# Optimization experiments

Measured on AMD Instinct MI355X. Metric: run time of the kernel, lower is better.

The kernel has to match this reference:

```python
import jax, jax.numpy as jnp
import numpy as np

B, H, L, D = 4, 16, 2048, 64


def setup_inputs() -> dict:
    key = jax.random.key(0)
    k1, k2, k3 = jax.random.split(key, 3)
    return {
        "query": jax.random.normal(k1, (B, H, L, D), dtype=jnp.float32),
        "key": jax.random.normal(k2, (B, H, L, D), dtype=jnp.float32),
        "value": jax.random.normal(k3, (B, H, D, L), dtype=jnp.float32),
    }


def reference(query, key, value):
    # dot_product_score = Q @ K^T / sqrt(D)   -> [B,H,L,L]
    d = query.shape[-1]
    scores = jnp.einsum("bhqd,bhkd->bhqk", query, key) / jnp.sqrt(jnp.asarray(d, query.dtype))
    attn = jax.nn.softmax(scores, axis=-1)
    # NOTE: original module returns matmul(value, attention_score) = V @ A
    # (value contracted over its last dim L with attn's query dim L) -> [B,H,D,L]
    return jnp.matmul(value, attn)
```

## Files before the change

### kernel.cpp

```cpp
#include <hip/hip_runtime.h>
#include <hip/hip_bf16.h>

#define L_SEQ 2048
#define D_HEAD 64
#define NHEADS 64
#define QSCALE (0.125f * 1.44269504088896340736f)

typedef __attribute__((ext_vector_type(8))) __bf16 bf16x8;
typedef __attribute__((ext_vector_type(16))) float f32x16;

__device__ __forceinline__ int swz(int row, int col) {
    int off = (row << 7) | (col << 1);
    return off ^ ((row & 7) << 4);
}
__device__ __forceinline__ bf16x8 read_frag(const char* lds, int row, int col) {
    return *reinterpret_cast<const bf16x8*>(lds + swz(row, col));
}

template <int ROWS>
__device__ __forceinline__ void stage_load(float4* regs, const float* src,
                                           int srcStride, int t) {
    int r0 = t >> 4, c4 = (t & 15) << 2;
#pragma unroll
    for (int i = 0; i < ROWS / 16; ++i)
        regs[i] = *reinterpret_cast<const float4*>(src + (size_t)(r0 + i * 16) * srcStride + c4);
}
template <int ROWS>
__device__ __forceinline__ void stage_write(char* lds, const float4* regs, int t,
                                            float scale) {
    int r0 = t >> 4, c4 = (t & 15) << 2;
#pragma unroll
    for (int i = 0; i < ROWS / 16; ++i) {
        float4 v = regs[i];
        union { __bf16 h[4]; unsigned long long u; } pk;
        pk.h[0] = (__bf16)(v.x * scale);
        pk.h[1] = (__bf16)(v.y * scale);
        pk.h[2] = (__bf16)(v.z * scale);
        pk.h[3] = (__bf16)(v.w * scale);
        *reinterpret_cast<unsigned long long*>(lds + swz(r0 + i * 16, c4)) = pk.u;
    }
}

__device__ __forceinline__ void pack_write(char* lds, int row, int c4, float4 v,
                                           float4 sc) {
    union { __bf16 h[4]; unsigned long long u; } pk;
    pk.h[0] = (__bf16)(v.x * sc.x);
    pk.h[1] = (__bf16)(v.y * sc.y);
    pk.h[2] = (__bf16)(v.z * sc.z);
    pk.h[3] = (__bf16)(v.w * sc.w);
    *reinterpret_cast<unsigned long long*>(lds + swz(row, c4)) = pk.u;
}

__device__ __forceinline__ unsigned cvt_pk_bf16(float lo, float hi) {
    unsigned r;
    asm("v_cvt_pk_bf16_f32 %0, %1, %2" : "=v"(r) : "v"(lo), "v"(hi));
    return r;
}

__global__ __launch_bounds__(256, 3) void attn_pass1(const float* __restrict__ Q,
                                                     const float* __restrict__ K,
                                                     float* __restrict__ invl) {
    __shared__ __align__(16) char lds[2][128 * 128];
    __shared__ float red[4][64];

    int bid = blockIdx.x;
    int sb = (bid & 7) * 256 + (bid >> 3);
    int bh = sb >> 5;
    int q0 = (sb & 31) << 6;
    const float* Qh = Q + (size_t)bh * L_SEQ * D_HEAD + (size_t)q0 * D_HEAD;
    const float* Kh = K + (size_t)bh * L_SEQ * D_HEAD;

    int t = threadIdx.x, lane = t & 63, w = t >> 6;
    int hl = lane >> 5, l31 = lane & 31;

    {
        float4 qreg[4];
        stage_load<64>(qreg, Qh, D_HEAD, t);
        stage_write<64>(lds[0], qreg, t, QSCALE);
    }
    __syncthreads();
    bf16x8 qfrag[2][4];
#pragma unroll
    for (int qb = 0; qb < 2; ++qb)
#pragma unroll
        for (int m = 0; m < 4; ++m)
            qfrag[qb][m] = read_frag(lds[0], qb * 32 + l31, m * 16 + hl * 8);
    __syncthreads();
    {
        float4 kreg[8];
        stage_load<128>(kreg, Kh, D_HEAD, t);
        stage_write<128>(lds[0], kreg, t, 1.0f);
    }
    __syncthreads();

    float lsum[2][16];
#pragma unroll
    for (int qb = 0; qb < 2; ++qb)
#pragma unroll
        for (int r = 0; r < 16; ++r) lsum[qb][r] = 0.f;

    for (int k0 = 0; k0 < L_SEQ; k0 += 128) {
        int c = (k0 >> 7) & 1;
        const char* kcur = lds[c];
        char* knext = lds[c ^ 1];

        int nk0 = (k0 + 128) & (L_SEQ - 1);
        float4 kreg[8];
        stage_load<128>(kreg, Kh + (size_t)nk0 * D_HEAD, D_HEAD, t);

        bf16x8 kfr[4];
#pragma unroll
        for (int m = 0; m < 4; ++m)
            kfr[m] = read_frag(kcur, w * 32 + l31, m * 16 + hl * 8);

        f32x16 s[2];
#pragma unroll
        for (int qb = 0; qb < 2; ++qb)
#pragma unroll
            for (int r = 0; r < 16; ++r) s[qb][r] = 0.f;

        __builtin_amdgcn_s_setprio(1);
#pragma unroll
        for (int m = 0; m < 4; ++m) {
            s[0] = __builtin_amdgcn_mfma_f32_32x32x16_bf16(qfrag[0][m], kfr[m], s[0], 0, 0, 0);
            s[1] = __builtin_amdgcn_mfma_f32_32x32x16_bf16(qfrag[1][m], kfr[m], s[1], 0, 0, 0);
        }
        __builtin_amdgcn_s_setprio(0);

#pragma unroll
        for (int qb = 0; qb < 2; ++qb)
#pragma unroll
            for (int r = 0; r < 16; ++r)
                lsum[qb][r] += __builtin_amdgcn_exp2f(s[qb][r]);

        stage_write<128>(knext, kreg, t, 1.0f);
        __syncthreads();
    }

#pragma unroll
    for (int qb = 0; qb < 2; ++qb)
#pragma unroll
        for (int r = 0; r < 16; ++r) {
            float v = lsum[qb][r];
            v += __shfl_xor(v, 1);
            v += __shfl_xor(v, 2);
            v += __shfl_xor(v, 4);
            v += __shfl_xor(v, 8);
            v += __shfl_xor(v, 16);
            lsum[qb][r] = v;
        }
    if (l31 == 0) {
#pragma unroll
        for (int qb = 0; qb < 2; ++qb)
#pragma unroll
            for (int r = 0; r < 16; ++r)
                red[w][qb * 32 + (r & 3) + 8 * (r >> 2) + 4 * hl] = lsum[qb][r];
    }
    __syncthreads();
    if (t < 64) {
        float ssum = red[0][t] + red[1][t] + red[2][t] + red[3][t];
        invl[(size_t)bh * L_SEQ + q0 + t] = 1.0f / ssum;
    }
}

__global__ __launch_bounds__(512, 4) void attn_pass2(const float* __restrict__ Q,
                                                     const float* __restrict__ K,
                                                     const float* __restrict__ V,
                                                     const float* __restrict__ invl,
                                                     float* __restrict__ out) {
    __shared__ __align__(16) char lds[32768];

    int bid = blockIdx.x;
    int sb = (bid & 7) * 64 + (bid >> 3);
    int bh = sb >> 3;
    int k0 = (sb & 7) << 8;
    const float* Qh = Q + (size_t)bh * L_SEQ * D_HEAD;
    const float* Kh = K + (size_t)bh * L_SEQ * D_HEAD + (size_t)k0 * D_HEAD;
    const float* Vh = V + (size_t)bh * D_HEAD * L_SEQ;
    const float* il = invl + (size_t)bh * L_SEQ;
    float* Oh = out + (size_t)bh * D_HEAD * L_SEQ;

    int t = threadIdx.x, lane = t & 63, w = t >> 6;
    int hl = lane >> 5, l31 = lane & 31;
    int r0 = t >> 4;
    int c4 = (t & 15) << 2;

#pragma unroll
    for (int i = 0; i < 8; ++i) {
        float4 v = *reinterpret_cast<const float4*>(Kh + (size_t)(r0 + i * 32) * D_HEAD + c4);
        pack_write(lds, r0 + i * 32, c4, v, make_float4(1.f, 1.f, 1.f, 1.f));
    }
    __syncthreads();
    bf16x8 kfrag[4];
#pragma unroll
    for (int m = 0; m < 4; ++m)
        kfrag[m] = read_frag(lds, w * 32 + l31, m * 16 + hl * 8);
    __syncthreads();

    {
        float4 qa = *reinterpret_cast<const float4*>(Qh + (size_t)r0 * D_HEAD + c4);
        float4 qb = *reinterpret_cast<const float4*>(Qh + (size_t)(r0 + 32) * D_HEAD + c4);
        float4 va = *reinterpret_cast<const float4*>(Vh + (size_t)r0 * L_SEQ + c4);
        float4 vb = *reinterpret_cast<const float4*>(Vh + (size_t)(r0 + 32) * L_SEQ + c4);
        float4 iv = *reinterpret_cast<const float4*>(il + c4);
        float4 qs = make_float4(QSCALE, QSCALE, QSCALE, QSCALE);
        pack_write(lds, r0, c4, qa, qs);
        pack_write(lds, r0 + 32, c4, qb, qs);
        pack_write(lds + 16384, r0, c4, va, iv);
        pack_write(lds + 16384, r0 + 32, c4, vb, iv);
    }
    __syncthreads();

    f32x16 acc[2];
#pragma unroll
    for (int db = 0; db < 2; ++db)
#pragma unroll
        for (int r = 0; r < 16; ++r) acc[db][r] = 0.f;

    for (int q0 = 0; q0 < L_SEQ; q0 += 64) {
        int c = (q0 >> 6) & 1;
        const char* qcur = c ? lds + 8192 : lds;
        const char* vcur = c ? lds + 24576 : lds + 16384;
        char* qnext = c ? lds : lds + 8192;
        char* vnext = c ? lds + 16384 : lds + 24576;

        int nq0 = (q0 + 64) & (L_SEQ - 1);
        float4 qra = *reinterpret_cast<const float4*>(Qh + (size_t)(nq0 + r0) * D_HEAD + c4);
        float4 qrb = *reinterpret_cast<const float4*>(Qh + (size_t)(nq0 + r0 + 32) * D_HEAD + c4);
        float4 vra = *reinterpret_cast<const float4*>(Vh + (size_t)r0 * L_SEQ + nq0 + c4);
        float4 vrb = *reinterpret_cast<const float4*>(Vh + (size_t)(r0 + 32) * L_SEQ + nq0 + c4);
        float4 ivn = *reinterpret_cast<const float4*>(il + nq0 + c4);

#pragma unroll
        for (int qq = 0; qq < 2; ++qq) {
            f32x16 s;
#pragma unroll
            for (int r = 0; r < 16; ++r) s[r] = 0.f;

            __builtin_amdgcn_s_setprio(1);
#pragma unroll
            for (int m = 0; m < 4; ++m) {
                bf16x8 afr = read_frag(qcur, qq * 32 + l31, m * 16 + hl * 8);
                s = __builtin_amdgcn_mfma_f32_32x32x16_bf16(afr, kfrag[m], s, 0, 0, 0);
            }
            __builtin_amdgcn_s_setprio(0);

            float p[16];
#pragma unroll
            for (int r = 0; r < 16; ++r) p[r] = __builtin_amdgcn_exp2f(s[r]);
            unsigned wA[4], wB[4];
#pragma unroll
            for (int g = 0; g < 4; ++g) {
                wA[g] = cvt_pk_bf16(p[4 * g + 0], p[4 * g + 1]);
                wB[g] = cvt_pk_bf16(p[4 * g + 2], p[4 * g + 3]);
            }
            bf16x8 pfrag[2];
#pragma unroll
            for (int mm = 0; mm < 2; ++mm) {
                unsigned a0 = wA[2 * mm], b0 = wA[2 * mm + 1];
                unsigned a1 = wB[2 * mm], b1 = wB[2 * mm + 1];
                asm volatile("v_permlane32_swap_b32 %0, %1" : "+v"(a0), "+v"(b0));
                asm volatile("v_permlane32_swap_b32 %0, %1" : "+v"(a1), "+v"(b1));
                union { unsigned u[4]; bf16x8 v; } pk;
                pk.u[0] = a0;
                pk.u[1] = a1;
                pk.u[2] = b0;
                pk.u[3] = b1;
                pfrag[mm] = pk.v;
            }

            __builtin_amdgcn_s_setprio(1);
#pragma unroll
            for (int mm = 0; mm < 2; ++mm)
#pragma unroll
                for (int db = 0; db < 2; ++db) {
                    bf16x8 vfr = read_frag(vcur, db * 32 + l31, qq * 32 + mm * 16 + hl * 8);
                    acc[db] = __builtin_amdgcn_mfma_f32_32x32x16_bf16(
                        vfr, pfrag[mm], acc[db], 0, 0, 0);
                }
            __builtin_amdgcn_s_setprio(0);
        }

        {
            float4 qs = make_float4(QSCALE, QSCALE, QSCALE, QSCALE);
            pack_write(qnext, r0, c4, qra, qs);
            pack_write(qnext, r0 + 32, c4, qrb, qs);
            pack_write(vnext, r0, c4, vra, ivn);
            pack_write(vnext, r0 + 32, c4, vrb, ivn);
        }
        __syncthreads();
    }

#pragma unroll
    for (int db = 0; db < 2; ++db)
#pragma unroll
        for (int r = 0; r < 16; ++r) {
            int d = db * 32 + (r & 3) + 8 * (r >> 2) + 4 * hl;
            int k = k0 + w * 32 + l31;
            Oh[(size_t)d * L_SEQ + k] = acc[db][r];
        }
}

extern "C" void kernel_launch(void* const* d_in, const int* in_sizes, int n_in,
                              void* d_out, int out_size, void* d_ws, size_t ws_size,
                              hipStream_t stream) {
    const float* Q = (const float*)d_in[0];
    const float* K = (const float*)d_in[1];
    const float* V = (const float*)d_in[2];
    float* invl = (float*)d_ws;
    float* out = (float*)d_out;

    attn_pass1<<<dim3(NHEADS * (L_SEQ / 64)), dim3(256), 0, stream>>>(Q, K, invl);
    attn_pass2<<<dim3(NHEADS * (L_SEQ / 256)), dim3(512), 0, stream>>>(Q, K, V, invl, out);
}
```

Measured before the change: 158.5 us.

## Retile both attention passes: larger Q tiles in pass1, 128-wide Q/V tiles in pass2

Pass1 now processes 128 query rows per block, split across a 2x2 wave grid, and iterates over 64-row K tiles. This halves the number of blocks and the total K traffic from global memory, and occupancy is raised to 4. Pass2 doubles the Q/V tile to 128 columns per iteration using 64KB of LDS with a new 256-byte-row swizzle for V, and it staggers the Q writes and V loads mid-iteration to overlap them with compute. The costs are more LDS per block and a more complex pipeline.

```diff
diff --git a/kernel.cpp b/kernel.cpp
--- a/kernel.cpp
+++ b/kernel.cpp
@@ -16,31 +16,6 @@
 __device__ __forceinline__ bf16x8 read_frag(const char* lds, int row, int col) {
     return *reinterpret_cast<const bf16x8*>(lds + swz(row, col));
 }
-
-template <int ROWS>
-__device__ __forceinline__ void stage_load(float4* regs, const float* src,
-                                           int srcStride, int t) {
-    int r0 = t >> 4, c4 = (t & 15) << 2;
-#pragma unroll
-    for (int i = 0; i < ROWS / 16; ++i)
-        regs[i] = *reinterpret_cast<const float4*>(src + (size_t)(r0 + i * 16) * srcStride + c4);
-}
-template <int ROWS>
-__device__ __forceinline__ void stage_write(char* lds, const float4* regs, int t,
-                                            float scale) {
-    int r0 = t >> 4, c4 = (t & 15) << 2;
-#pragma unroll
-    for (int i = 0; i < ROWS / 16; ++i) {
-        float4 v = regs[i];
-        union { __bf16 h[4]; unsigned long long u; } pk;
-        pk.h[0] = (__bf16)(v.x * scale);
-        pk.h[1] = (__bf16)(v.y * scale);
-        pk.h[2] = (__bf16)(v.z * scale);
-        pk.h[3] = (__bf16)(v.w * scale);
-        *reinterpret_cast<unsigned long long*>(lds + swz(r0 + i * 16, c4)) = pk.u;
-    }
-}
-
 __device__ __forceinline__ void pack_write(char* lds, int row, int c4, float4 v,
                                            float4 sc) {
     union { __bf16 h[4]; unsigned long long u; } pk;
@@ -51,32 +26,55 @@
     *reinterpret_cast<unsigned long long*>(lds + swz(row, c4)) = pk.u;
 }
 
+__device__ __forceinline__ int swz128(int row, int col) {
+    int off = (row << 8) | (col << 1);
+    return off ^ ((row & 15) << 4);
+}
+__device__ __forceinline__ bf16x8 read_frag128(const char* lds, int row, int col) {
+    return *reinterpret_cast<const bf16x8*>(lds + swz128(row, col));
+}
+__device__ __forceinline__ void pack_write128(char* lds, int row, int c4, float4 v,
+                                              float4 sc) {
+    union { __bf16 h[4]; unsigned long long u; } pk;
+    pk.h[0] = (__bf16)(v.x * sc.x);
+    pk.h[1] = (__bf16)(v.y * sc.y);
+    pk.h[2] = (__bf16)(v.z * sc.z);
+    pk.h[3] = (__bf16)(v.w * sc.w);
+    *reinterpret_cast<unsigned long long*>(lds + swz128(row, c4)) = pk.u;
+}
+
 __device__ __forceinline__ unsigned cvt_pk_bf16(float lo, float hi) {
     unsigned r;
     asm("v_cvt_pk_bf16_f32 %0, %1, %2" : "=v"(r) : "v"(lo), "v"(hi));
     return r;
 }
 
-__global__ __launch_bounds__(256, 3) void attn_pass1(const float* __restrict__ Q,
+__global__ __launch_bounds__(256, 4) void attn_pass1(const float* __restrict__ Q,
                                                      const float* __restrict__ K,
                                                      float* __restrict__ invl) {
-    __shared__ __align__(16) char lds[2][128 * 128];
-    __shared__ float red[4][64];
+    __shared__ __align__(16) char lds[16384];
+    __shared__ float red[2][128];
 
     int bid = blockIdx.x;
-    int sb = (bid & 7) * 256 + (bid >> 3);
-    int bh = sb >> 5;
-    int q0 = (sb & 31) << 6;
+    int sb = (bid & 7) * 128 + (bid >> 3);
+    int bh = sb >> 4;
+    int q0 = (sb & 15) << 7;
     const float* Qh = Q + (size_t)bh * L_SEQ * D_HEAD + (size_t)q0 * D_HEAD;
     const float* Kh = K + (size_t)bh * L_SEQ * D_HEAD;
 
     int t = threadIdx.x, lane = t & 63, w = t >> 6;
+    int wq = w >> 1, wk = w & 1;
     int hl = lane >> 5, l31 = lane & 31;
+    int r0 = t >> 4;
+    int c4 = (t & 15) << 2;
 
     {
-        float4 qreg[4];
-        stage_load<64>(qreg, Qh, D_HEAD, t);
-        stage_write<64>(lds[0], qreg, t, QSCALE);
+        float4 qs = make_float4(QSCALE, QSCALE, QSCALE, QSCALE);
+#pragma unroll
+        for (int i = 0; i < 8; ++i) {
+            float4 v = *reinterpret_cast<const float4*>(Qh + (size_t)(r0 + i * 16) * D_HEAD + c4);
+            pack_write(lds, r0 + i * 16, c4, v, qs);
+        }
     }
     __syncthreads();
     bf16x8 qfrag[2][4];
@@ -84,12 +82,15 @@
     for (int qb = 0; qb < 2; ++qb)
 #pragma unroll
         for (int m = 0; m < 4; ++m)
-            qfrag[qb][m] = read_frag(lds[0], qb * 32 + l31, m * 16 + hl * 8);
+            qfrag[qb][m] = read_frag(lds, wq * 64 + qb * 32 + l31, m * 16 + hl * 8);
     __syncthreads();
     {
-        float4 kreg[8];
-        stage_load<128>(kreg, Kh, D_HEAD, t);
-        stage_write<128>(lds[0], kreg, t, 1.0f);
+        float4 one = make_float4(1.f, 1.f, 1.f, 1.f);
+#pragma unroll
+        for (int i = 0; i < 4; ++i) {
+            float4 v = *reinterpret_cast<const float4*>(Kh + (size_t)(r0 + i * 16) * D_HEAD + c4);
+            pack_write(lds, r0 + i * 16, c4, v, one);
+        }
     }
     __syncthreads();
 
@@ -99,41 +100,43 @@
 #pragma unroll
         for (int r = 0; r < 16; ++r) lsum[qb][r] = 0.f;
 
-    for (int k0 = 0; k0 < L_SEQ; k0 += 128) {
-        int c = (k0 >> 7) & 1;
-        const char* kcur = lds[c];
-        char* knext = lds[c ^ 1];
-
-        int nk0 = (k0 + 128) & (L_SEQ - 1);
-        float4 kreg[8];
-        stage_load<128>(kreg, Kh + (size_t)nk0 * D_HEAD, D_HEAD, t);
+    for (int k0 = 0; k0 < L_SEQ; k0 += 64) {
+        int c = (k0 >> 6) & 1;
+        const char* kcur = lds + (c ? 8192 : 0);
+        char* knext = lds + (c ? 0 : 8192);
+
+        int nk0 = (k0 + 64) & (L_SEQ - 1);
+        float4 kreg[4];
+#pragma unroll
+        for (int i = 0; i < 4; ++i)
+            kreg[i] = *reinterpret_cast<const float4*>(Kh + (size_t)(nk0 + r0 + i * 16) * D_HEAD + c4);
 
         bf16x8 kfr[4];
 #pragma unroll
         for (int m = 0; m < 4; ++m)
-            kfr[m] = read_frag(kcur, w * 32 + l31, m * 16 + hl * 8);
-
-        f32x16 s[2];
-#pragma unroll
-        for (int qb = 0; qb < 2; ++qb)
-#pragma unroll
-            for (int r = 0; r < 16; ++r) s[qb][r] = 0.f;
+            kfr[m] = read_frag(kcur, wk * 32 + l31, m * 16 + hl * 8);
 
         __builtin_amdgcn_s_setprio(1);
 #pragma unroll
-        for (int m = 0; m < 4; ++m) {
-            s[0] = __builtin_amdgcn_mfma_f32_32x32x16_bf16(qfrag[0][m], kfr[m], s[0], 0, 0, 0);
-            s[1] = __builtin_amdgcn_mfma_f32_32x32x16_bf16(qfrag[1][m], kfr[m], s[1], 0, 0, 0);
+        for (int qb = 0; qb < 2; ++qb) {
+            f32x16 s;
+#pragma unroll
+            for (int r = 0; r < 16; ++r) s[r] = 0.f;
+#pragma unroll
+            for (int m = 0; m < 4; ++m)
+                s = __builtin_amdgcn_mfma_f32_32x32x16_bf16(qfrag[qb][m], kfr[m], s, 0, 0, 0);
+#pragma unroll
+            for (int r = 0; r < 16; ++r)
+                lsum[qb][r] += __builtin_amdgcn_exp2f(s[r]);
         }
         __builtin_amdgcn_s_setprio(0);
 
-#pragma unroll
-        for (int qb = 0; qb < 2; ++qb)
-#pragma unroll
-            for (int r = 0; r < 16; ++r)
-                lsum[qb][r] += __builtin_amdgcn_exp2f(s[qb][r]);
-
-        stage_write<128>(knext, kreg, t, 1.0f);
+        {
+            float4 one = make_float4(1.f, 1.f, 1.f, 1.f);
+#pragma unroll
+            for (int i = 0; i < 4; ++i)
+                pack_write(knext, r0 + i * 16, c4, kreg[i], one);
+        }
         __syncthreads();
     }
 
@@ -154,11 +157,11 @@
         for (int qb = 0; qb < 2; ++qb)
 #pragma unroll
             for (int r = 0; r < 16; ++r)
-                red[w][qb * 32 + (r & 3) + 8 * (r >> 2) + 4 * hl] = lsum[qb][r];
-    }
-    __syncthreads();
-    if (t < 64) {
-        float ssum = red[0][t] + red[1][t] + red[2][t] + red[3][t];
+                red[wk][wq * 64 + qb * 32 + (r & 3) + 8 * (r >> 2) + 4 * hl] = lsum[qb][r];
+    }
+    __syncthreads();
+    if (t < 128) {
+        float ssum = red[0][t] + red[1][t];
         invl[(size_t)bh * L_SEQ + q0 + t] = 1.0f / ssum;
     }
 }
@@ -168,7 +171,7 @@
                                                      const float* __restrict__ V,
                                                      const float* __restrict__ invl,
                                                      float* __restrict__ out) {
-    __shared__ __align__(16) char lds[32768];
+    __shared__ __align__(16) char lds[65536];
 
     int bid = blockIdx.x;
     int sb = (bid & 7) * 64 + (bid >> 3);
@@ -184,11 +187,16 @@
     int hl = lane >> 5, l31 = lane & 31;
     int r0 = t >> 4;
     int c4 = (t & 15) << 2;
-
-#pragma unroll
-    for (int i = 0; i < 8; ++i) {
-        float4 v = *reinterpret_cast<const float4*>(Kh + (size_t)(r0 + i * 32) * D_HEAD + c4);
-        pack_write(lds, r0 + i * 32, c4, v, make_float4(1.f, 1.f, 1.f, 1.f));
+    int r0v = t >> 5;
+    int c8 = (t & 31) << 2;
+
+    {
+        float4 one = make_float4(1.f, 1.f, 1.f, 1.f);
+#pragma unroll
+        for (int i = 0; i < 8; ++i) {
+            float4 v = *reinterpret_cast<const float4*>(Kh + (size_t)(r0 + i * 32) * D_HEAD + c4);
+            pack_write(lds, r0 + i * 32, c4, v, one);
+        }
     }
     __syncthreads();
     bf16x8 kfrag[4];
@@ -198,16 +206,18 @@
     __syncthreads();
 
     {
-        float4 qa = *reinterpret_cast<const float4*>(Qh + (size_t)r0 * D_HEAD + c4);
-        float4 qb = *reinterpret_cast<const float4*>(Qh + (size_t)(r0 + 32) * D_HEAD + c4);
-        float4 va = *reinterpret_cast<const float4*>(Vh + (size_t)r0 * L_SEQ + c4);
-        float4 vb = *reinterpret_cast<const float4*>(Vh + (size_t)(r0 + 32) * L_SEQ + c4);
-        float4 iv = *reinterpret_cast<const float4*>(il + c4);
         float4 qs = make_float4(QSCALE, QSCALE, QSCALE, QSCALE);
-        pack_write(lds, r0, c4, qa, qs);
-        pack_write(lds, r0 + 32, c4, qb, qs);
-        pack_write(lds + 16384, r0, c4, va, iv);
-        pack_write(lds + 16384, r0 + 32, c4, vb, iv);
+#pragma unroll
+        for (int i = 0; i < 4; ++i) {
+            float4 v = *reinterpret_cast<const float4*>(Qh + (size_t)(r0 + i * 32) * D_HEAD + c4);
+            pack_write(lds, r0 + i * 32, c4, v, qs);
+        }
+        float4 iv = *reinterpret_cast<const float4*>(il + c8);
+#pragma unroll
+        for (int i = 0; i < 4; ++i) {
+            float4 v = *reinterpret_cast<const float4*>(Vh + (size_t)(r0v + i * 16) * L_SEQ + c8);
+            pack_write128(lds + 16384, r0v + i * 16, c8, v, iv);
+        }
     }
     __syncthreads();
 
@@ -217,26 +227,25 @@
 #pragma unroll
         for (int r = 0; r < 16; ++r) acc[db][r] = 0.f;
 
-    for (int q0 = 0; q0 < L_SEQ; q0 += 64) {
-        int c = (q0 >> 6) & 1;
-        const char* qcur = c ? lds + 8192 : lds;
-        const char* vcur = c ? lds + 24576 : lds + 16384;
-        char* qnext = c ? lds : lds + 8192;
-        char* vnext = c ? lds + 16384 : lds + 24576;
-
-        int nq0 = (q0 + 64) & (L_SEQ - 1);
-        float4 qra = *reinterpret_cast<const float4*>(Qh + (size_t)(nq0 + r0) * D_HEAD + c4);
-        float4 qrb = *reinterpret_cast<const float4*>(Qh + (size_t)(nq0 + r0 + 32) * D_HEAD + c4);
-        float4 vra = *reinterpret_cast<const float4*>(Vh + (size_t)r0 * L_SEQ + nq0 + c4);
-        float4 vrb = *reinterpret_cast<const float4*>(Vh + (size_t)(r0 + 32) * L_SEQ + nq0 + c4);
-        float4 ivn = *reinterpret_cast<const float4*>(il + nq0 + c4);
-
-#pragma unroll
-        for (int qq = 0; qq < 2; ++qq) {
+    for (int q0 = 0; q0 < L_SEQ; q0 += 128) {
+        int c = (q0 >> 7) & 1;
+        const char* qcur = lds + (c ? 32768 : 0);
+        const char* vcur = qcur + 16384;
+        char* qnext = lds + (c ? 0 : 32768);
+        char* vnext = qnext + 16384;
+
+        int nq0 = (q0 + 128) & (L_SEQ - 1);
+        float4 qreg[4];
+#pragma unroll
+        for (int i = 0; i < 4; ++i)
+            qreg[i] = *reinterpret_cast<const float4*>(Qh + (size_t)(nq0 + r0 + i * 32) * D_HEAD + c4);
+        float4 vreg[4], ivn;
+
+#pragma unroll
+        for (int qq = 0; qq < 4; ++qq) {
             f32x16 s;
 #pragma unroll
             for (int r = 0; r < 16; ++r) s[r] = 0.f;
-
             __builtin_amdgcn_s_setprio(1);
 #pragma unroll
             for (int m = 0; m < 4; ++m) {
@@ -245,14 +254,13 @@
             }
             __builtin_amdgcn_s_setprio(0);
 
-            float p[16];
-#pragma unroll
-            for (int r = 0; r < 16; ++r) p[r] = __builtin_amdgcn_exp2f(s[r]);
             unsigned wA[4], wB[4];
 #pragma unroll
             for (int g = 0; g < 4; ++g) {
-                wA[g] = cvt_pk_bf16(p[4 * g + 0], p[4 * g + 1]);
-                wB[g] = cvt_pk_bf16(p[4 * g + 2], p[4 * g + 3]);
+                wA[g] = cvt_pk_bf16(__builtin_amdgcn_exp2f(s[4 * g + 0]),
+                                    __builtin_amdgcn_exp2f(s[4 * g + 1]));
+                wB[g] = cvt_pk_bf16(__builtin_amdgcn_exp2f(s[4 * g + 2]),
+                                    __builtin_amdgcn_exp2f(s[4 * g + 3]));
             }
             bf16x8 pfrag[2];
 #pragma unroll
@@ -274,20 +282,26 @@
             for (int mm = 0; mm < 2; ++mm)
 #pragma unroll
                 for (int db = 0; db < 2; ++db) {
-                    bf16x8 vfr = read_frag(vcur, db * 32 + l31, qq * 32 + mm * 16 + hl * 8);
+                    bf16x8 vfr = read_frag128(vcur, db * 32 + l31, qq * 32 + mm * 16 + hl * 8);
                     acc[db] = __builtin_amdgcn_mfma_f32_32x32x16_bf16(
                         vfr, pfrag[mm], acc[db], 0, 0, 0);
                 }
             __builtin_amdgcn_s_setprio(0);
-        }
-
-        {
-            float4 qs = make_float4(QSCALE, QSCALE, QSCALE, QSCALE);
-            pack_write(qnext, r0, c4, qra, qs);
-            pack_write(qnext, r0 + 32, c4, qrb, qs);
-            pack_write(vnext, r0, c4, vra, ivn);
-            pack_write(vnext, r0 + 32, c4, vrb, ivn);
-        }
+
+            if (qq == 1) {
+                float4 qs = make_float4(QSCALE, QSCALE, QSCALE, QSCALE);
+#pragma unroll
+                for (int i = 0; i < 4; ++i)
+                    pack_write(qnext, r0 + i * 32, c4, qreg[i], qs);
+#pragma unroll
+                for (int i = 0; i < 4; ++i)
+                    vreg[i] = *reinterpret_cast<const float4*>(Vh + (size_t)(r0v + i * 16) * L_SEQ + nq0 + c8);
+                ivn = *reinterpret_cast<const float4*>(il + nq0 + c8);
+            }
+        }
+#pragma unroll
+        for (int i = 0; i < 4; ++i)
+            pack_write128(vnext, r0v + i * 16, c8, vreg[i], ivn);
         __syncthreads();
     }
 
@@ -310,6 +324,6 @@
     float* invl = (float*)d_ws;
     float* out = (float*)d_out;
 
-    attn_pass1<<<dim3(NHEADS * (L_SEQ / 64)), dim3(256), 0, stream>>>(Q, K, invl);
+    attn_pass1<<<dim3(NHEADS * (L_SEQ / 128)), dim3(256), 0, stream>>>(Q, K, invl);
     attn_pass2<<<dim3(NHEADS * (L_SEQ / 256)), dim3(512), 0, stream>>>(Q, K, V, invl, out);
 }
```

Result: faster. 139.6 us (-11.9%).
